# Kernel tuning notes

Hardware: AMD Instinct MI355X
Metric: run time of the kernel (lower is better)

## Reference

```python
import jax, jax.numpy as jnp
import numpy as np

B, C, H, W = 32, 256, 64, 64
M, D = 256, 512           # memory_size, memory_dim
NH, HD = 8, 64            # heads, head_dim
EPS = 1e-5


def setup_inputs() -> dict:
    key = jax.random.key(0)
    ks = jax.random.split(key, 12)
    s = 0.02
    return {
        "x": jax.random.normal(ks[0], (B, C, H, W), jnp.float32),
        "memory_bank": jax.random.normal(ks[1], (M, D), jnp.float32),
        "enc_conv_w": jax.random.normal(ks[2], (D // 2, C), jnp.float32) * s,  # 1x1 conv == channel matmul
        "enc_conv_b": jnp.zeros((D // 2,), jnp.float32),
        "bn_gamma": jnp.ones((D // 2,), jnp.float32),
        "bn_beta": jnp.zeros((D // 2,), jnp.float32),
        "bn_mean": jnp.zeros((D // 2,), jnp.float32),
        "bn_var": jnp.ones((D // 2,), jnp.float32),
        "enc_lin_w": jax.random.normal(ks[3], (D, D // 2), jnp.float32) * s,
        "enc_lin_b": jnp.zeros((D,), jnp.float32),
        "ln_gamma": jnp.ones((D,), jnp.float32),
        "ln_beta": jnp.zeros((D,), jnp.float32),
        "attn_in_w": jax.random.normal(ks[4], (3 * D, D), jnp.float32) * s,
        "attn_in_b": jnp.zeros((3 * D,), jnp.float32),
        "attn_out_w": jax.random.normal(ks[5], (D, D), jnp.float32) * s,
        "attn_out_b": jnp.zeros((D,), jnp.float32),
        "gate_w": jax.random.normal(ks[6], (D, 2 * D), jnp.float32) * s,
        "gate_b": jnp.zeros((D,), jnp.float32),
        "rec_w1": jax.random.normal(ks[7], (D // 2, D), jnp.float32) * s,
        "rec_b1": jnp.zeros((D // 2,), jnp.float32),
        "rec_w2": jax.random.normal(ks[8], (C, D // 2), jnp.float32) * s,
        "rec_b2": jnp.zeros((C,), jnp.float32),
        "spat_conv_w": jax.random.normal(ks[9], (1, 2, 7, 7), jnp.float32) * s,
    }


def reference(x, memory_bank, enc_conv_w, enc_conv_b, bn_gamma, bn_beta, bn_mean, bn_var,
              enc_lin_w, enc_lin_b, ln_gamma, ln_beta, attn_in_w, attn_in_b,
              attn_out_w, attn_out_b, gate_w, gate_b, rec_w1, rec_b1, rec_w2, rec_b2,
              spat_conv_w):
    # ---- feature encoder: 1x1 conv -> BN(eval) -> ReLU -> global avg pool -> Linear -> LayerNorm ----
    h = jnp.einsum('bchw,oc->bohw', x, enc_conv_w) + enc_conv_b[None, :, None, None]
    bn_scale = (bn_gamma / jnp.sqrt(bn_var + EPS))[None, :, None, None]
    h = (h - bn_mean[None, :, None, None]) * bn_scale + bn_beta[None, :, None, None]
    h = jax.nn.relu(h)
    h = h.mean(axis=(2, 3))                                   # (B, D//2)
    h = h @ enc_lin_w.T + enc_lin_b                           # (B, D)
    mu = h.mean(-1, keepdims=True)
    var = h.var(-1, keepdims=True)
    enc = (h - mu) / jnp.sqrt(var + EPS) * ln_gamma + ln_beta  # (B, D)

    # ---- memory retrieval: MHA with q_len=1, keys/values = shared memory bank ----
    Wq, Wk, Wv = jnp.split(attn_in_w, 3, axis=0)
    bq, bk, bv = jnp.split(attn_in_b, 3)
    q = (enc @ Wq.T + bq).reshape(B, NH, HD)                  # (B, H, d)
    k = (memory_bank @ Wk.T + bk).reshape(M, NH, HD)          # (M, H, d) — batch-shared
    v = (memory_bank @ Wv.T + bv).reshape(M, NH, HD)
    scores = jnp.einsum('bhd,mhd->bhm', q, k) / np.float32(np.sqrt(HD))
    att = jax.nn.softmax(scores, axis=-1)                     # (B, H, M)
    ctx = jnp.einsum('bhm,mhd->bhd', att, v).reshape(B, D)
    retrieved = ctx @ attn_out_w.T + attn_out_b               # (B, D)

    # ---- gated fusion ----
    gate = jax.nn.sigmoid(jnp.concatenate([enc, retrieved], axis=-1) @ gate_w.T + gate_b)
    fused = gate * enc + (1.0 - gate) * retrieved             # (B, D)

    # ---- per-channel weights from fused features ----
    sw = jax.nn.sigmoid(jax.nn.relu(fused @ rec_w1.T + rec_b1) @ rec_w2.T + rec_b2)  # (B, C)

    # ---- spatial attention on [avg, max] channel stats ----
    avg = x.mean(axis=1, keepdims=True)
    mx = x.max(axis=1, keepdims=True)
    sp_in = jnp.concatenate([avg, mx], axis=1)                # (B, 2, H, W)
    sa = jax.lax.conv_general_dilated(sp_in, spat_conv_w, (1, 1), [(3, 3), (3, 3)],
                                      dimension_numbers=('NCHW', 'OIHW', 'NCHW'))
    sa = jax.nn.sigmoid(sa)                                   # (B, 1, H, W)

    return x * sw[:, :, None, None] * sa                      # (B, C, H, W)
```

## Files before the change

kernel.cpp:

```cpp
#include <hip/hip_runtime.h>
#include <math.h>

#define EPSV 1e-5f

typedef __attribute__((ext_vector_type(8))) short short8;
typedef __attribute__((ext_vector_type(8))) unsigned short ushort8;
typedef __attribute__((ext_vector_type(4))) float f32x4;

__device__ __forceinline__ unsigned short f2bf(float f){
  unsigned u = __builtin_bit_cast(unsigned, f);
  u += 0x7fffu + ((u >> 16) & 1u);
  return (unsigned short)(u >> 16);
}
__device__ __forceinline__ float dot4f(float4 w, const float* v){
  return w.x*v[0] + w.y*v[1] + w.z*v[2] + w.w*v[3];
}
__device__ __forceinline__ float sigmoidf(float v){ return 1.f/(1.f + expf(-v)); }

__global__ __launch_bounds__(256) void k_pack(const float* __restrict__ w1,
                                              const float* __restrict__ wattn,
                                              unsigned short* __restrict__ p1,
                                              unsigned short* __restrict__ pkv){
  const int total1 = 256*256, total2 = 1024*512;
  for (int idx = blockIdx.x*256 + threadIdx.x; idx < total1 + total2; idx += gridDim.x*256){
    if (idx < total1){
      int o = idx >> 8, c = idx & 255;
      int off = (((o>>4)*8 + (c>>5))*64 + (((c>>3)&3)*16 + (o&15)))*8 + (c&7);
      p1[off] = f2bf(w1[idx]);
    } else {
      int j = idx - total1; int o = j >> 9, c = j & 511;
      int off = (((o>>4)*16 + (c>>5))*64 + (((c>>3)&3)*16 + (o&15)))*8 + (c&7);
      pkv[off] = f2bf(wattn[512*512 + j]);
    }
  }
}

__global__ __launch_bounds__(256) void k_conv(
    const float* __restrict__ x, const unsigned short* __restrict__ wp,
    const float* __restrict__ cb, const float* __restrict__ bng,
    const float* __restrict__ bnb, const float* __restrict__ bnm,
    const float* __restrict__ bnv,
    float* __restrict__ ppool, float* __restrict__ wavg, float* __restrict__ wmax){
  int bid = blockIdx.x;
  int b = bid >> 6, tile = bid & 63;
  int px0 = tile << 6;
  int t = threadIdx.x;
  int lane = t & 63, wv = t >> 6;
  int px = t & 63, cg = wv;
  __shared__ __align__(16) unsigned short a_lds[2048];
  __shared__ float st_s[256], st_m[256];

  const float* xb = x + (size_t)b*(256*4096) + px0 + px;

  f32x4 acc[4][4];
  #pragma unroll
  for (int i = 0; i < 4; ++i)
    #pragma unroll
    for (int j = 0; j < 4; ++j){ f32x4 z = {0.f,0.f,0.f,0.f}; acc[i][j] = z; }

  float ssum = 0.f, smax = -3.4e38f;
  const unsigned awoff = ((px >> 4) << 9) + (((unsigned)cg << 4) + (px & 15)) * 8;

  for (int ch = 0; ch < 8; ++ch){
    float xv[8];
    #pragma unroll
    for (int u = 0; u < 8; ++u)
      xv[u] = xb[(size_t)(ch*32 + cg*8 + u) * 4096];
    ushort8 pk;
    #pragma unroll
    for (int u = 0; u < 8; ++u){
      ssum += xv[u];
      smax = fmaxf(smax, xv[u]);
      pk[u] = f2bf(xv[u]);
    }
    __syncthreads();
    *(ushort8*)(a_lds + awoff) = pk;
    __syncthreads();
    short8 afr[4];
    #pragma unroll
    for (int mf = 0; mf < 4; ++mf) afr[mf] = *(const short8*)(a_lds + (mf << 9) + lane*8);
    #pragma unroll
    for (int nf = 0; nf < 4; ++nf){
      short8 bfr = *(const short8*)(wp + (size_t)(((wv*4 + nf)*8 + ch) * 512 + lane*8));
      #pragma unroll
      for (int mf = 0; mf < 4; ++mf)
        acc[mf][nf] = __builtin_amdgcn_mfma_f32_16x16x32_bf16(afr[mf], bfr, acc[mf][nf], 0, 0, 0);
    }
  }

  st_s[t] = ssum; st_m[t] = smax;
  __syncthreads();
  if (t < 64){
    float s = st_s[t] + st_s[t+64] + st_s[t+128] + st_s[t+192];
    float m = fmaxf(fmaxf(st_m[t], st_m[t+64]), fmaxf(st_m[t+128], st_m[t+192]));
    wavg[(b << 12) + px0 + t] = s * (1.f/256.f);
    wmax[(b << 12) + px0 + t] = m;
  }

  #pragma unroll
  for (int nf = 0; nf < 4; ++nf){
    int o = (wv << 6) + (nf << 4) + (lane & 15);
    float sc = bng[o] * rsqrtf(bnv[o] + EPSV);
    float sh = bnb[o] + (cb[o] - bnm[o]) * sc;
    float ps = 0.f;
    #pragma unroll
    for (int mf = 0; mf < 4; ++mf)
      #pragma unroll
      for (int r = 0; r < 4; ++r)
        ps += fmaxf(acc[mf][nf][r] * sc + sh, 0.f);
    ps += __shfl_xor(ps, 16, 64);
    ps += __shfl_xor(ps, 32, 64);
    if ((lane & 48) == 0)
      ppool[(size_t)((b << 6) + tile)*256 + o] = ps;
  }
}

__global__ __launch_bounds__(256) void k_enc(const float* __restrict__ pp,
    const float* __restrict__ lw, const float* __restrict__ lb,
    const float* __restrict__ lng, const float* __restrict__ lnb,
    float* __restrict__ enc){
  int b = blockIdx.x, t = threadIdx.x;
  __shared__ __align__(16) float p_s[256];
  __shared__ float h_s[512], red[8];
  float s = 0.f;
  for (int tile = 0; tile < 64; ++tile) s += pp[(size_t)((b<<6)+tile)*256 + t];
  p_s[t] = s * (1.f/4096.f);
  __syncthreads();
  float hv[2];
  #pragma unroll
  for (int k = 0; k < 2; ++k){
    int d = t + k*256;
    const float4* wr = (const float4*)(lw + (size_t)d*256);
    float a = 0.f;
    for (int j = 0; j < 64; ++j) a += dot4f(wr[j], &p_s[4*j]);
    hv[k] = a + lb[d];
    h_s[d] = hv[k];
  }
  float ls = hv[0] + hv[1], lq = hv[0]*hv[0] + hv[1]*hv[1];
  #pragma unroll
  for (int msk = 1; msk < 64; msk <<= 1){
    ls += __shfl_xor(ls, msk, 64);
    lq += __shfl_xor(lq, msk, 64);
  }
  if ((t & 63) == 0){ red[t>>6] = ls; red[4 + (t>>6)] = lq; }
  __syncthreads();
  float su = red[0]+red[1]+red[2]+red[3];
  float sq = red[4]+red[5]+red[6]+red[7];
  float mu = su * (1.f/512.f);
  float vr = sq * (1.f/512.f) - mu*mu;
  float rstd = rsqrtf(vr + EPSV);
  #pragma unroll
  for (int k = 0; k < 2; ++k){
    int d = t + k*256;
    enc[(size_t)b*512 + d] = (h_s[d] - mu)*rstd*lng[d] + lnb[d];
  }
}

__global__ __launch_bounds__(256) void k_kv(const float* __restrict__ mb,
    const unsigned short* __restrict__ wp, const float* __restrict__ attb,
    float* __restrict__ kvb){
  int bid = blockIdx.x;
  int mu = bid & 1, nt = (bid >> 1) & 7, mt = bid >> 4;
  int m0 = mt << 6, n0 = nt << 6;
  int t = threadIdx.x, lane = t & 63, wv = t >> 6;
  int ml = t & 63, cg = wv;
  __shared__ __align__(16) unsigned short a_lds[2048];

  f32x4 acc[4];
  #pragma unroll
  for (int i = 0; i < 4; ++i){ f32x4 z = {0.f,0.f,0.f,0.f}; acc[i] = z; }

  const unsigned awoff = ((ml >> 4) << 9) + (((unsigned)cg << 4) + (ml & 15))*8;
  int ofrag = mu*32 + (n0 >> 4) + wv;
  float bias = attb[512 + mu*512 + n0 + (wv << 4) + (lane & 15)];

  for (int ch = 0; ch < 16; ++ch){
    const float4* src = (const float4*)(mb + (size_t)(m0 + ml)*512 + ch*32 + cg*8);
    float4 v0 = src[0], v1 = src[1];
    ushort8 pk;
    pk[0]=f2bf(v0.x); pk[1]=f2bf(v0.y); pk[2]=f2bf(v0.z); pk[3]=f2bf(v0.w);
    pk[4]=f2bf(v1.x); pk[5]=f2bf(v1.y); pk[6]=f2bf(v1.z); pk[7]=f2bf(v1.w);
    __syncthreads();
    *(ushort8*)(a_lds + awoff) = pk;
    __syncthreads();
    short8 bfr = *(const short8*)(wp + (size_t)(ofrag*16 + ch)*512 + lane*8);
    #pragma unroll
    for (int mf = 0; mf < 4; ++mf){
      short8 afr = *(const short8*)(a_lds + (mf << 9) + lane*8);
      acc[mf] = __builtin_amdgcn_mfma_f32_16x16x32_bf16(afr, bfr, acc[mf], 0, 0, 0);
    }
  }
  #pragma unroll
  for (int mf = 0; mf < 4; ++mf)
    #pragma unroll
    for (int r = 0; r < 4; ++r){
      int row = m0 + (mf << 4) + ((lane >> 4) << 2) + r;
      int col = n0 + (wv << 4) + (lane & 15);
      kvb[(size_t)mu*131072 + (size_t)row*512 + col] = acc[mf][r] + bias;
    }
}

__global__ __launch_bounds__(256) void k_qkattn(const float* __restrict__ enc,
    const float* __restrict__ kvb, const float* __restrict__ attw,
    const float* __restrict__ attb, float* __restrict__ ctxout){
  int bid = blockIdx.x;
  int b = bid >> 3, h = bid & 7;
  int t = threadIdx.x;
  __shared__ float e_s[512];
  __shared__ __align__(16) float q_s[64];
  __shared__ float att_s[256];
  __shared__ float red_s[256];
  __shared__ float r2[8];

  e_s[t]       = enc[(size_t)b*512 + t];
  e_s[t + 256] = enc[(size_t)b*512 + 256 + t];
  __syncthreads();

  {
    int i = t >> 2, part = t & 3;
    const float4* wr = (const float4*)(attw + (size_t)(h*64 + i)*512 + part*128);
    const float* ev = e_s + part*128;
    float a = 0.f;
    #pragma unroll
    for (int j = 0; j < 32; ++j) a += dot4f(wr[j], ev + 4*j);
    a += __shfl_xor(a, 1, 64);
    a += __shfl_xor(a, 2, 64);
    if (part == 0) q_s[i] = a + attb[h*64 + i];
  }
  __syncthreads();

  float sc;
  {
    const float4* kr = (const float4*)(kvb + (size_t)t*512 + h*64);
    const float4* qr = (const float4*)q_s;
    float a = 0.f;
    #pragma unroll
    for (int j = 0; j < 16; ++j){
      float4 kk = kr[j], qq = qr[j];
      a += kk.x*qq.x + kk.y*qq.y + kk.z*qq.z + kk.w*qq.w;
    }
    sc = a * 0.125f;
  }
  int wv = t >> 6, lane = t & 63;
  float mx = sc;
  #pragma unroll
  for (int msk = 1; msk < 64; msk <<= 1) mx = fmaxf(mx, __shfl_xor(mx, msk, 64));
  if (lane == 0) r2[wv] = mx;
  __syncthreads();
  mx = fmaxf(fmaxf(r2[0], r2[1]), fmaxf(r2[2], r2[3]));
  float ex = expf(sc - mx);
  float sum = ex;
  #pragma unroll
  for (int msk = 1; msk < 64; msk <<= 1) sum += __shfl_xor(sum, msk, 64);
  if (lane == 0) r2[4 + wv] = sum;
  __syncthreads();
  float inv = 1.f / (r2[4] + r2[5] + r2[6] + r2[7]);
  att_s[t] = ex * inv;
  __syncthreads();

  {
    const float* vbase = kvb + 131072 + (size_t)(wv*64)*512 + h*64 + lane;
    const float* at = att_s + wv*64;
    float a = 0.f;
    #pragma unroll 8
    for (int m = 0; m < 64; ++m) a += at[m] * vbase[(size_t)m*512];
    red_s[wv*64 + lane] = a;
  }
  __syncthreads();
  if (t < 64)
    ctxout[(size_t)b*512 + h*64 + t] = red_s[t] + red_s[64+t] + red_s[128+t] + red_s[192+t];
}

__global__ __launch_bounds__(256) void k_outproj(const float* __restrict__ ctx,
    const float* __restrict__ ow, const float* __restrict__ obv,
    float* __restrict__ retr){
  int bid = blockIdx.x;
  int b = bid >> 3, n0 = (bid & 7) << 6;
  int t = threadIdx.x;
  __shared__ float c_s[512];
  c_s[t]       = ctx[(size_t)b*512 + t];
  c_s[t + 256] = ctx[(size_t)b*512 + 256 + t];
  __syncthreads();
  int o = n0 + (t >> 2), part = t & 3;
  const float4* wr = (const float4*)(ow + (size_t)o*512 + part*128);
  const float* cv = c_s + part*128;
  float a = 0.f;
  #pragma unroll
  for (int j = 0; j < 32; ++j) a += dot4f(wr[j], cv + 4*j);
  a += __shfl_xor(a, 1, 64);
  a += __shfl_xor(a, 2, 64);
  if (part == 0) retr[(size_t)b*512 + o] = a + obv[o];
}

__global__ __launch_bounds__(256) void k_gate(const float* __restrict__ enc,
    const float* __restrict__ retr, const float* __restrict__ gw,
    const float* __restrict__ gb, float* __restrict__ fused){
  int bid = blockIdx.x;
  int b = bid >> 3, n0 = (bid & 7) << 6;
  int t = threadIdx.x;
  __shared__ float ef[1024];
  ef[t]        = enc[(size_t)b*512 + t];
  ef[t + 256]  = enc[(size_t)b*512 + 256 + t];
  ef[t + 512]  = retr[(size_t)b*512 + t];
  ef[t + 768]  = retr[(size_t)b*512 + 256 + t];
  __syncthreads();
  int o = n0 + (t >> 2), part = t & 3;
  const float4* wr = (const float4*)(gw + (size_t)o*1024 + part*256);
  const float* fv = ef + part*256;
  float a = 0.f;
  #pragma unroll
  for (int j = 0; j < 64; ++j) a += dot4f(wr[j], fv + 4*j);
  a += __shfl_xor(a, 1, 64);
  a += __shfl_xor(a, 2, 64);
  if (part == 0){
    float g = sigmoidf(a + gb[o]);
    fused[(size_t)b*512 + o] = g*ef[o] + (1.f - g)*ef[512 + o];
  }
}

__global__ __launch_bounds__(256) void k_rec1(const float* __restrict__ fused,
    const float* __restrict__ r1w, const float* __restrict__ r1b,
    float* __restrict__ t1){
  int bid = blockIdx.x;
  int b = bid >> 2, n0 = (bid & 3) << 6;
  int t = threadIdx.x;
  __shared__ float f_s[512];
  f_s[t]       = fused[(size_t)b*512 + t];
  f_s[t + 256] = fused[(size_t)b*512 + 256 + t];
  __syncthreads();
  int o = n0 + (t >> 2), part = t & 3;
  const float4* wr = (const float4*)(r1w + (size_t)o*512 + part*128);
  const float* fv = f_s + part*128;
  float a = 0.f;
  #pragma unroll
  for (int j = 0; j < 32; ++j) a += dot4f(wr[j], fv + 4*j);
  a += __shfl_xor(a, 1, 64);
  a += __shfl_xor(a, 2, 64);
  if (part == 0) t1[(size_t)b*256 + o] = fmaxf(a + r1b[o], 0.f);
}

__global__ __launch_bounds__(256) void k_rec2(const float* __restrict__ t1,
    const float* __restrict__ r2w, const float* __restrict__ r2b,
    float* __restrict__ swout){
  int bid = blockIdx.x;
  int b = bid >> 2, n0 = (bid & 3) << 6;
  int t = threadIdx.x;
  __shared__ float t_s[256];
  t_s[t] = t1[(size_t)b*256 + t];
  __syncthreads();
  int o = n0 + (t >> 2), part = t & 3;
  const float4* wr = (const float4*)(r2w + (size_t)o*256 + part*64);
  const float* tv = t_s + part*64;
  float a = 0.f;
  #pragma unroll
  for (int j = 0; j < 16; ++j) a += dot4f(wr[j], tv + 4*j);
  a += __shfl_xor(a, 1, 64);
  a += __shfl_xor(a, 2, 64);
  if (part == 0) swout[(size_t)b*256 + o] = sigmoidf(a + r2b[o]);
}

__global__ __launch_bounds__(256) void k_spconv(const float* __restrict__ wavg,
    const float* __restrict__ wmax, const float* __restrict__ wgt,
    float* __restrict__ sa){
  __shared__ float w_s[98];
  int t = threadIdx.x;
  if (t < 98) w_s[t] = wgt[t];
  __syncthreads();
  int b = blockIdx.x >> 4;
  int px = ((blockIdx.x & 15) << 8) + t;
  int y = px >> 6, xx = px & 63;
  const float* pa = wavg + (b << 12);
  const float* pm = wmax + (b << 12);
  float a = 0.f;
  #pragma unroll
  for (int ky = 0; ky < 7; ++ky){
    int yy = y + ky - 3;
    if (yy < 0 || yy >= 64) continue;
    #pragma unroll
    for (int kx = 0; kx < 7; ++kx){
      int x2 = xx + kx - 3;
      if (x2 < 0 || x2 >= 64) continue;
      int o = (yy << 6) + x2;
      a += pa[o]*w_s[ky*7+kx] + pm[o]*w_s[49+ky*7+kx];
    }
  }
  sa[(b << 12) + px] = sigmoidf(a);
}

__global__ __launch_bounds__(256) void k_final(const float* __restrict__ x,
    const float* __restrict__ sw, const float* __restrict__ sa,
    float* __restrict__ out){
  const size_t total = 8388608;
  for (size_t q = (size_t)blockIdx.x*256 + threadIdx.x; q < total; q += (size_t)gridDim.x*256){
    size_t b = q >> 18;
    int c = (int)((q >> 10) & 255);
    int p4 = (int)(q & 1023);
    float4 xv = ((const float4*)x)[q];
    float4 sv = ((const float4*)sa)[(b << 10) + p4];
    float s = sw[(b << 8) + c];
    float4 o;
    o.x = xv.x * s * sv.x;
    o.y = xv.y * s * sv.y;
    o.z = xv.z * s * sv.z;
    o.w = xv.w * s * sv.w;
    ((float4*)out)[q] = o;
  }
}

extern "C" void kernel_launch(void* const* d_in, const int* in_sizes, int n_in,
                              void* d_out, int out_size, void* d_ws, size_t ws_size,
                              hipStream_t stream){
  const float* x    = (const float*)d_in[0];
  const float* mb   = (const float*)d_in[1];
  const float* w1   = (const float*)d_in[2];
  const float* cbv  = (const float*)d_in[3];
  const float* bng  = (const float*)d_in[4];
  const float* bnb  = (const float*)d_in[5];
  const float* bnm  = (const float*)d_in[6];
  const float* bnv  = (const float*)d_in[7];
  const float* lw   = (const float*)d_in[8];
  const float* lb   = (const float*)d_in[9];
  const float* lng  = (const float*)d_in[10];
  const float* lnb  = (const float*)d_in[11];
  const float* attw = (const float*)d_in[12];
  const float* attb = (const float*)d_in[13];
  const float* ow   = (const float*)d_in[14];
  const float* obv  = (const float*)d_in[15];
  const float* gw   = (const float*)d_in[16];
  const float* gb   = (const float*)d_in[17];
  const float* r1w  = (const float*)d_in[18];
  const float* r1b  = (const float*)d_in[19];
  const float* r2w  = (const float*)d_in[20];
  const float* r2b  = (const float*)d_in[21];
  const float* spw  = (const float*)d_in[22];
  float* out = (float*)d_out;

  char* ws = (char*)d_ws;
  unsigned short* w1p  = (unsigned short*)(ws + 0);
  unsigned short* wkvp = (unsigned short*)(ws + 131072);
  float* ppool = (float*)(ws + 1179648);
  float* wavg  = (float*)(ws + 3276800);
  float* wmax  = (float*)(ws + 3801088);
  float* encb  = (float*)(ws + 4325376);
  float* kvb   = (float*)(ws + 4390912);
  float* swb   = (float*)(ws + 5439488);
  float* sab   = (float*)(ws + 5472256);
  float* ctxb  = (float*)(ws + 5996544);
  float* retrb = (float*)(ws + 6062080);
  float* fusedb= (float*)(ws + 6127616);
  float* t1b   = (float*)(ws + 6193152);

  k_pack   <<<2304, 256, 0, stream>>>(w1, attw, w1p, wkvp);
  k_conv   <<<2048, 256, 0, stream>>>(x, w1p, cbv, bng, bnb, bnm, bnv, ppool, wavg, wmax);
  k_enc    <<<32,   256, 0, stream>>>(ppool, lw, lb, lng, lnb, encb);
  k_kv     <<<64,   256, 0, stream>>>(mb, wkvp, attb, kvb);
  k_qkattn <<<256,  256, 0, stream>>>(encb, kvb, attw, attb, ctxb);
  k_outproj<<<256,  256, 0, stream>>>(ctxb, ow, obv, retrb);
  k_gate   <<<256,  256, 0, stream>>>(encb, retrb, gw, gb, fusedb);
  k_rec1   <<<128,  256, 0, stream>>>(fusedb, r1w, r1b, t1b);
  k_rec2   <<<128,  256, 0, stream>>>(t1b, r2w, r2b, swb);
  k_spconv <<<512,  256, 0, stream>>>(wavg, wmax, spw, sab);
  k_final  <<<2048, 256, 0, stream>>>(x, swb, sab, out);
}
```

Before: 189.1 us.

## Stage full conv input tile in LDS once; split KV projection into smaller blocks

The conv kernel now loads all 8 channel chunks of its 64-pixel tile into a larger 32KB LDS buffer in one pass with a single barrier, then runs all MFMAs afterward. This removes the two barriers per chunk and lets the global loads issue back to back. The KV projection kernel drops LDS staging and loads bf16 A fragments straight from global memory, using 256 blocks of 16 rows each instead of 64 blocks. The cost is more LDS per block, which may lower occupancy in the conv kernel, and more redundant reads of the memory bank in the KV kernel.

```diff
diff --git a/kernel.cpp b/kernel.cpp
--- a/kernel.cpp
+++ b/kernel.cpp
@@ -47,20 +47,15 @@
   int t = threadIdx.x;
   int lane = t & 63, wv = t >> 6;
   int px = t & 63, cg = wv;
-  __shared__ __align__(16) unsigned short a_lds[2048];
+  __shared__ __align__(16) unsigned short a_lds[16384];
   __shared__ float st_s[256], st_m[256];
 
   const float* xb = x + (size_t)b*(256*4096) + px0 + px;
 
-  f32x4 acc[4][4];
-  #pragma unroll
-  for (int i = 0; i < 4; ++i)
-    #pragma unroll
-    for (int j = 0; j < 4; ++j){ f32x4 z = {0.f,0.f,0.f,0.f}; acc[i][j] = z; }
-
   float ssum = 0.f, smax = -3.4e38f;
-  const unsigned awoff = ((px >> 4) << 9) + (((unsigned)cg << 4) + (px & 15)) * 8;
-
+  const unsigned wbase = (((px >> 4) << 6) + ((unsigned)cg << 4) + (px & 15)) << 4;
+
+  #pragma unroll
   for (int ch = 0; ch < 8; ++ch){
     float xv[8];
     #pragma unroll
@@ -73,12 +68,30 @@
       smax = fmaxf(smax, xv[u]);
       pk[u] = f2bf(xv[u]);
     }
-    __syncthreads();
-    *(ushort8*)(a_lds + awoff) = pk;
-    __syncthreads();
+    *(ushort8*)((char*)a_lds + wbase + (ch << 12)) = pk;
+  }
+  st_s[t] = ssum; st_m[t] = smax;
+  __syncthreads();
+
+  if (t < 64){
+    float s = st_s[t] + st_s[t+64] + st_s[t+128] + st_s[t+192];
+    float m = fmaxf(fmaxf(st_m[t], st_m[t+64]), fmaxf(st_m[t+128], st_m[t+192]));
+    wavg[(b << 12) + px0 + t] = s * (1.f/256.f);
+    wmax[(b << 12) + px0 + t] = m;
+  }
+
+  f32x4 acc[4][4];
+  #pragma unroll
+  for (int i = 0; i < 4; ++i)
+    #pragma unroll
+    for (int j = 0; j < 4; ++j){ f32x4 z = {0.f,0.f,0.f,0.f}; acc[i][j] = z; }
+
+  #pragma unroll
+  for (int ch = 0; ch < 8; ++ch){
     short8 afr[4];
     #pragma unroll
-    for (int mf = 0; mf < 4; ++mf) afr[mf] = *(const short8*)(a_lds + (mf << 9) + lane*8);
+    for (int mf = 0; mf < 4; ++mf)
+      afr[mf] = *(const short8*)((const char*)a_lds + (ch << 12) + (mf << 10) + lane*16);
     #pragma unroll
     for (int nf = 0; nf < 4; ++nf){
       short8 bfr = *(const short8*)(wp + (size_t)(((wv*4 + nf)*8 + ch) * 512 + lane*8));
@@ -86,15 +99,6 @@
       for (int mf = 0; mf < 4; ++mf)
         acc[mf][nf] = __builtin_amdgcn_mfma_f32_16x16x32_bf16(afr[mf], bfr, acc[mf][nf], 0, 0, 0);
     }
-  }
-
-  st_s[t] = ssum; st_m[t] = smax;
-  __syncthreads();
-  if (t < 64){
-    float s = st_s[t] + st_s[t+64] + st_s[t+128] + st_s[t+192];
-    float m = fmaxf(fmaxf(st_m[t], st_m[t+64]), fmaxf(st_m[t+128], st_m[t+192]));
-    wavg[(b << 12) + px0 + t] = s * (1.f/256.f);
-    wmax[(b << 12) + px0 + t] = m;
   }
 
   #pragma unroll
@@ -160,44 +164,36 @@
     const unsigned short* __restrict__ wp, const float* __restrict__ attb,
     float* __restrict__ kvb){
   int bid = blockIdx.x;
-  int mu = bid & 1, nt = (bid >> 1) & 7, mt = bid >> 4;
-  int m0 = mt << 6, n0 = nt << 6;
+  int mt = bid >> 4, nt = bid & 15;
+  int m0 = mt << 4;
+  int mu = nt >> 3;
+  int ncol0 = (nt & 7) << 6;
   int t = threadIdx.x, lane = t & 63, wv = t >> 6;
-  int ml = t & 63, cg = wv;
-  __shared__ __align__(16) unsigned short a_lds[2048];
-
-  f32x4 acc[4];
-  #pragma unroll
-  for (int i = 0; i < 4; ++i){ f32x4 z = {0.f,0.f,0.f,0.f}; acc[i] = z; }
-
-  const unsigned awoff = ((ml >> 4) << 9) + (((unsigned)cg << 4) + (ml & 15))*8;
-  int ofrag = mu*32 + (n0 >> 4) + wv;
-  float bias = attb[512 + mu*512 + n0 + (wv << 4) + (lane & 15)];
-
+  int l15 = lane & 15, l4 = lane >> 4;
+
+  const float* arow = mb + (size_t)(m0 + l15)*512 + l4*8;
+  int ofrag = (nt << 2) + wv;
+
+  f32x4 acc = {0.f,0.f,0.f,0.f};
+  #pragma unroll
   for (int ch = 0; ch < 16; ++ch){
-    const float4* src = (const float4*)(mb + (size_t)(m0 + ml)*512 + ch*32 + cg*8);
-    float4 v0 = src[0], v1 = src[1];
-    ushort8 pk;
-    pk[0]=f2bf(v0.x); pk[1]=f2bf(v0.y); pk[2]=f2bf(v0.z); pk[3]=f2bf(v0.w);
-    pk[4]=f2bf(v1.x); pk[5]=f2bf(v1.y); pk[6]=f2bf(v1.z); pk[7]=f2bf(v1.w);
-    __syncthreads();
-    *(ushort8*)(a_lds + awoff) = pk;
-    __syncthreads();
+    float4 a0 = *(const float4*)(arow + ch*32);
+    float4 a1 = *(const float4*)(arow + ch*32 + 4);
+    short8 afr;
+    afr[0] = (short)f2bf(a0.x); afr[1] = (short)f2bf(a0.y);
+    afr[2] = (short)f2bf(a0.z); afr[3] = (short)f2bf(a0.w);
+    afr[4] = (short)f2bf(a1.x); afr[5] = (short)f2bf(a1.y);
+    afr[6] = (short)f2bf(a1.z); afr[7] = (short)f2bf(a1.w);
     short8 bfr = *(const short8*)(wp + (size_t)(ofrag*16 + ch)*512 + lane*8);
-    #pragma unroll
-    for (int mf = 0; mf < 4; ++mf){
-      short8 afr = *(const short8*)(a_lds + (mf << 9) + lane*8);
-      acc[mf] = __builtin_amdgcn_mfma_f32_16x16x32_bf16(afr, bfr, acc[mf], 0, 0, 0);
-    }
-  }
-  #pragma unroll
-  for (int mf = 0; mf < 4; ++mf)
-    #pragma unroll
-    for (int r = 0; r < 4; ++r){
-      int row = m0 + (mf << 4) + ((lane >> 4) << 2) + r;
-      int col = n0 + (wv << 4) + (lane & 15);
-      kvb[(size_t)mu*131072 + (size_t)row*512 + col] = acc[mf][r] + bias;
-    }
+    acc = __builtin_amdgcn_mfma_f32_16x16x32_bf16(afr, bfr, acc, 0, 0, 0);
+  }
+  float bias = attb[512 + mu*512 + ncol0 + (wv << 4) + l15];
+  #pragma unroll
+  for (int i = 0; i < 4; ++i){
+    int row = m0 + l4*4 + i;
+    int col = ncol0 + (wv << 4) + l15;
+    kvb[(size_t)mu*131072 + (size_t)row*512 + col] = acc[i] + bias;
+  }
 }
 
 __global__ __launch_bounds__(256) void k_qkattn(const float* __restrict__ enc,
@@ -453,7 +449,7 @@
   k_pack   <<<2304, 256, 0, stream>>>(w1, attw, w1p, wkvp);
   k_conv   <<<2048, 256, 0, stream>>>(x, w1p, cbv, bng, bnb, bnm, bnv, ppool, wavg, wmax);
   k_enc    <<<32,   256, 0, stream>>>(ppool, lw, lb, lng, lnb, encb);
-  k_kv     <<<64,   256, 0, stream>>>(mb, wkvp, attb, kvb);
+  k_kv     <<<256,  256, 0, stream>>>(mb, wkvp, attb, kvb);
   k_qkattn <<<256,  256, 0, stream>>>(encb, kvb, attw, attb, ctxb);
   k_outproj<<<256,  256, 0, stream>>>(ctxb, ow, obv, retrb);
   k_gate   <<<256,  256, 0, stream>>>(encb, retrb, gw, gb, fusedb);
```

New measurement: 179.3 us. 5.2% less time.
